# Kernel tuning notes

Measured on AMD Instinct MI355X. Metric: run time of the kernel, lower is better.

The kernel has to match this reference:

```python
import jax, jax.numpy as jnp
import numpy as np

B, L, D, H = 4, 2048, 1024, 16
HD = D // H

def setup_inputs() -> dict:
    key = jax.random.key(0)
    ks = jax.random.split(key, 11)
    s = 1.0 / np.sqrt(D)
    return {
        "query": jax.random.normal(ks[0], (B, L, D), jnp.float32),
        "key": jax.random.normal(ks[1], (B, L, D), jnp.float32),
        "value": jax.random.normal(ks[2], (B, L, D), jnp.float32),
        "Wq": jax.random.normal(ks[3], (D, D), jnp.float32) * s,
        "bq": jnp.zeros((D,), jnp.float32),
        "Wk": jax.random.normal(ks[4], (D, D), jnp.float32) * s,
        "bk": jnp.zeros((D,), jnp.float32),
        "Wv": jax.random.normal(ks[5], (D, D), jnp.float32) * s,
        "bv": jnp.zeros((D,), jnp.float32),
        "Wo": jax.random.normal(ks[6], (D, D), jnp.float32) * s,
        "bo": jnp.zeros((D,), jnp.float32),
    }

def reference(query, key, value, Wq, bq, Wk, bk, Wv, bv, Wo, bo):
    b = query.shape[0]
    # linear projections (torch Linear: x @ W.T + b)
    Q = query @ Wq.T + bq
    K = key @ Wk.T + bk
    V = value @ Wv.T + bv
    # split heads -> [b, h, l, hd]
    Q = Q.reshape(b, -1, H, HD).transpose(0, 2, 1, 3)
    K = K.reshape(b, -1, H, HD).transpose(0, 2, 1, 3)
    V = V.reshape(b, -1, H, HD).transpose(0, 2, 1, 3)
    energy = jnp.einsum('bhqd,bhkd->bhqk', Q, K) / jnp.sqrt(jnp.float32(HD))
    attn = jax.nn.softmax(energy, axis=-1)
    x = jnp.einsum('bhqk,bhkd->bhqd', attn, V)
    x = x.transpose(0, 2, 1, 3).reshape(b, -1, D)
    return x @ Wo.T + bo
```

## Files before the change

### kernel.cpp

```cpp
#include <hip/hip_runtime.h>

typedef float floatx4 __attribute__((ext_vector_type(4)));
typedef short bf16x8 __attribute__((ext_vector_type(8)));
typedef const unsigned int __attribute__((address_space(1))) gas_u32;
typedef unsigned int __attribute__((address_space(3))) las_u32;

#if __has_builtin(__builtin_amdgcn_exp2f)
#define EXP2F(x) __builtin_amdgcn_exp2f(x)
#else
#define EXP2F(x) exp2f(x)
#endif

__device__ __forceinline__ unsigned short f2bf(float x) {
    unsigned int u = __float_as_uint(x);
    unsigned int r = u + 0x7fffu + ((u >> 16) & 1u);
    return (unsigned short)(r >> 16);
}

__device__ __forceinline__ unsigned int pack2bf_t(float lo, float hi) {
    return (__float_as_uint(lo) >> 16) | (__float_as_uint(hi) & 0xffff0000u);
}

__device__ __forceinline__ void g2l16(const void* g, void* l) {
    __builtin_amdgcn_global_load_lds((gas_u32*)(unsigned long long)g,
                                     (las_u32*)(unsigned int)(unsigned long long)l,
                                     16, 0, 0);
}

__global__ __launch_bounds__(256) void cvt5_kernel(
    const float* __restrict__ k, const float* __restrict__ v,
    const float* __restrict__ wq, const float* __restrict__ wk, const float* __restrict__ wv,
    unsigned short* __restrict__ kb, unsigned short* __restrict__ vb,
    unsigned short* __restrict__ wqb, unsigned short* __restrict__ wkb,
    unsigned short* __restrict__ wvb) {
    const int ty = blockIdx.y;
    const float* src; unsigned short* dst; int n4;
    switch (ty) {
        case 0: src = k;  dst = kb;  n4 = 2097152; break;
        case 1: src = v;  dst = vb;  n4 = 2097152; break;
        case 2: src = wq; dst = wqb; n4 = 262144;  break;
        case 3: src = wk; dst = wkb; n4 = 262144;  break;
        default: src = wv; dst = wvb; n4 = 262144; break;
    }
    int i = blockIdx.x * 256 + threadIdx.x;
    if (i >= n4) return;
    float4 x = ((const float4*)src)[i];
    ushort4 o;
    o.x = f2bf(x.x); o.y = f2bf(x.y); o.z = f2bf(x.z); o.w = f2bf(x.w);
    ((ushort4*)dst)[i] = o;
}

__global__ __launch_bounds__(256) void cvt1_kernel(const float* __restrict__ wo,
                                                   unsigned short* __restrict__ wob) {
    int i = blockIdx.x * 256 + threadIdx.x;
    float4 x = ((const float4*)wo)[i];
    ushort4 o;
    o.x = f2bf(x.x); o.y = f2bf(x.y); o.z = f2bf(x.z); o.w = f2bf(x.w);
    ((ushort4*)wob)[i] = o;
}

template <int OUT_MODE, bool A_FP32>
__device__ __forceinline__ void gemm_body(const void* __restrict__ Aptr,
                                          const unsigned short* __restrict__ W,
                                          const float* __restrict__ bias,
                                          void* __restrict__ Cout,
                                          unsigned short* As, unsigned short* Bs,
                                          int m0, int n0, int N, int K, float scale) {
    const int t = threadIdx.x;
    const int lane = t & 63, w = t >> 6;
    const int lr = lane & 15, quad = lane >> 4;
    const int wm = (w & 1) * 64, wn = (w >> 1) * 64;

    const int s0 = w * 128 + lane, s1 = s0 + 64;
    const int r0 = s0 >> 2, c0 = ((s0 & 3) ^ (r0 & 3)) * 8;
    const int r1 = s1 >> 2, c1 = ((s1 & 3) ^ (r1 & 3)) * 8;
    const unsigned short* gw0 = W + (size_t)(n0 + r0) * K + c0;
    const unsigned short* gw1 = W + (size_t)(n0 + r1) * K + c1;

    const unsigned short* ga0 = nullptr;
    const unsigned short* ga1 = nullptr;
    if constexpr (!A_FP32) {
        const unsigned short* A = (const unsigned short*)Aptr;
        ga0 = A + (size_t)(m0 + r0) * K + c0;
        ga1 = A + (size_t)(m0 + r1) * K + c1;
    }

    floatx4 acc[4][4];
#pragma unroll
    for (int i = 0; i < 4; ++i)
#pragma unroll
        for (int j = 0; j < 4; ++j) acc[i][j] = (floatx4){0.f, 0.f, 0.f, 0.f};

    const int xs = (lr & 3);

    auto stageB = [&](int buf, int k0) {
        unsigned short* Bb = Bs + buf * 4096;
        g2l16(gw0 + k0, &Bb[(size_t)(w * 128) * 8]);
        g2l16(gw1 + k0, &Bb[(size_t)(w * 128 + 64) * 8]);
    };

    auto readB = [&](int buf, bf16x8* bfr, int ch) {
        const unsigned short* Bb = Bs + buf * 4096;
#pragma unroll
        for (int j = 0; j < 4; ++j)
            bfr[j] = *(const bf16x8*)&Bb[(wn + j * 16 + lr) * 32 + ch * 8];
    };

    auto mfma16 = [&](const bf16x8* af, const bf16x8* bfr) {
#pragma unroll
        for (int i = 0; i < 4; ++i)
#pragma unroll
            for (int j = 0; j < 4; ++j) {
                if constexpr (OUT_MODE == 2)
                    acc[i][j] = __builtin_amdgcn_mfma_f32_16x16x32_bf16(bfr[j], af[i], acc[i][j], 0, 0, 0);
                else
                    acc[i][j] = __builtin_amdgcn_mfma_f32_16x16x32_bf16(af[i], bfr[j], acc[i][j], 0, 0, 0);
            }
    };

    if constexpr (!A_FP32) {
        auto stageA = [&](int buf, int k0) {
            unsigned short* Ab = As + buf * 4096;
            g2l16(ga0 + k0, &Ab[(size_t)(w * 128) * 8]);
            g2l16(ga1 + k0, &Ab[(size_t)(w * 128 + 64) * 8]);
        };
        auto step = [&](int buf) {
            const unsigned short* Ab = As + buf * 4096;
            bf16x8 af[4], bfr[4];
#pragma unroll
            for (int i = 0; i < 4; ++i)
                af[i] = *(const bf16x8*)&Ab[(wm + i * 16 + lr) * 32 + ((quad ^ xs) * 8)];
            readB(buf, bfr, quad ^ xs);
            mfma16(af, bfr);
        };
        stageB(0, 0);
        stageA(0, 0);
        __syncthreads();
        for (int k0 = 0; k0 < K - 64; k0 += 64) {
            stageB(1, k0 + 32);
            stageA(1, k0 + 32);
            step(0);
            __syncthreads();
            stageB(0, k0 + 64);
            stageA(0, k0 + 64);
            step(1);
            __syncthreads();
        }
        stageB(1, K - 32);
        stageA(1, K - 32);
        step(0);
        __syncthreads();
        step(1);
    } else {
        const float* A = (const float*)Aptr;
        float4 va[4];
        auto loadA32 = [&](int k0) {
#pragma unroll
            for (int i = 0; i < 4; ++i) {
                int idx = t + 256 * i;
                int row = idx >> 3;
                int c4 = (idx & 7) * 4;
                va[i] = *(const float4*)(A + (size_t)(m0 + row) * K + k0 + c4);
            }
        };
        auto writeA32 = [&](int buf) {
            unsigned short* Ab = As + buf * 4096;
#pragma unroll
            for (int i = 0; i < 4; ++i) {
                int idx = t + 256 * i;
                int row = idx >> 3;
                int c4 = (idx & 7) * 4;
                ushort4 bv;
                bv.x = f2bf(va[i].x); bv.y = f2bf(va[i].y);
                bv.z = f2bf(va[i].z); bv.w = f2bf(va[i].w);
                *(ushort4*)&Ab[row * 32 + c4] = bv;
            }
        };
        auto stepA = [&](int buf) {
            const unsigned short* Ab = As + buf * 4096;
            bf16x8 af[4], bfr[4];
#pragma unroll
            for (int i = 0; i < 4; ++i)
                af[i] = *(const bf16x8*)&Ab[(wm + i * 16 + lr) * 32 + quad * 8];
            readB(buf, bfr, quad ^ xs);
            mfma16(af, bfr);
        };
        stageB(0, 0);
        loadA32(0);
        writeA32(0);
        __syncthreads();
        for (int k0 = 0; k0 < K - 64; k0 += 64) {
            stageB(1, k0 + 32);
            loadA32(k0 + 32);
            stepA(0);
            writeA32(1);
            __syncthreads();
            stageB(0, k0 + 64);
            loadA32(k0 + 64);
            stepA(1);
            writeA32(0);
            __syncthreads();
        }
        stageB(1, K - 32);
        loadA32(K - 32);
        stepA(0);
        writeA32(1);
        __syncthreads();
        stepA(1);
    }

    if constexpr (OUT_MODE == 2) {
        const int b = m0 >> 11;
        unsigned short* VT = (unsigned short*)Cout;
#pragma unroll
        for (int i = 0; i < 4; ++i) {
#pragma unroll
            for (int j = 0; j < 4; ++j) {
#pragma unroll
                for (int r = 0; r < 4; ++r) {
                    int d = n0 + wn + j * 16 + quad * 4 + r;
                    int tok = (m0 & 2047) + wm + i * 16 + lr;
                    float val = acc[i][j][r] + bias[d];
                    int t6 = tok & 63;
                    int ntok = (tok & ~63) | ((((t6 >> 3) ^ (d & 7)) << 3)) | (t6 & 7);
                    VT[(((size_t)b * 16 + (d >> 6)) * 64 + (d & 63)) * 2048 + ntok] = f2bf(val);
                }
            }
        }
    } else if constexpr (OUT_MODE == 3) {
        unsigned short* C = (unsigned short*)Cout;
#pragma unroll
        for (int i = 0; i < 4; ++i) {
#pragma unroll
            for (int j = 0; j < 4; ++j) {
#pragma unroll
                for (int r = 0; r < 4; ++r) {
                    int row = m0 + wm + i * 16 + quad * 4 + r;
                    int col = n0 + wn + j * 16 + lr;
                    float val = acc[i][j][r] + bias[col];
                    int r6 = row & 63;
                    int srow = (r6 & 32) | (((r6 >> 2) & 1) << 4) |
                               (((r6 >> 3) & 3) << 2) | (r6 & 3);
                    int nrow = (row & ~63) | srow;
                    int c6 = col & 63;
                    int ncol = (col & ~63) | ((((c6 >> 3) ^ (srow & 7)) << 3)) | (c6 & 7);
                    C[(size_t)nrow * N + ncol] = f2bf(val);
                }
            }
        }
    } else {
#pragma unroll
        for (int i = 0; i < 4; ++i) {
#pragma unroll
            for (int j = 0; j < 4; ++j) {
#pragma unroll
                for (int r = 0; r < 4; ++r) {
                    int row = m0 + wm + i * 16 + quad * 4 + r;
                    int col = n0 + wn + j * 16 + lr;
                    float val = (acc[i][j][r] + bias[col]) * scale;
                    if constexpr (OUT_MODE == 1)
                        ((unsigned short*)Cout)[(size_t)row * N + col] = f2bf(val);
                    else
                        ((float*)Cout)[(size_t)row * N + col] = val;
                }
            }
        }
    }
}

__device__ __forceinline__ void gemm_swz(int bx, int by, int& m0, int& n0) {
    const int hw = bx + 8 * by;
    const int wid = (hw & 7) * 64 + (hw >> 3);
    m0 = (wid >> 3) * 128;
    n0 = (wid & 7) * 128;
}

__global__ __launch_bounds__(256) void gemm_qkv(
    const float* __restrict__ query, const unsigned short* __restrict__ wqb,
    const float* __restrict__ bq, unsigned short* __restrict__ Qp,
    const unsigned short* __restrict__ kb, const unsigned short* __restrict__ wkb,
    const float* __restrict__ bk, unsigned short* __restrict__ Kp,
    const unsigned short* __restrict__ vb, const unsigned short* __restrict__ wvb,
    const float* __restrict__ bv, unsigned short* __restrict__ VTp, float qscale) {
    __shared__ unsigned short As[2 * 128 * 32];
    __shared__ unsigned short Bs[2 * 128 * 32];
    int m0, n0;
    gemm_swz(blockIdx.x, blockIdx.y, m0, n0);
    if (blockIdx.z == 0)
        gemm_body<1, true>(query, wqb, bq, Qp, As, Bs, m0, n0, 1024, 1024, qscale);
    else if (blockIdx.z == 1)
        gemm_body<3, false>(kb, wkb, bk, Kp, As, Bs, m0, n0, 1024, 1024, 1.0f);
    else
        gemm_body<2, false>(vb, wvb, bv, VTp, As, Bs, m0, n0, 1024, 1024, 1.0f);
}

__global__ __launch_bounds__(256) void gemm_o(const unsigned short* __restrict__ A,
                                              const unsigned short* __restrict__ W,
                                              const float* __restrict__ bias,
                                              void* __restrict__ C) {
    __shared__ unsigned short As[2 * 128 * 32];
    __shared__ unsigned short Bs[2 * 128 * 32];
    int m0, n0;
    gemm_swz(blockIdx.x, blockIdx.y, m0, n0);
    gemm_body<0, false>(A, W, bias, C, As, Bs, m0, n0, 1024, 1024, 1.0f);
}

__global__ __launch_bounds__(256) void attn_kernel(const unsigned short* __restrict__ Qp,
                                                   const unsigned short* __restrict__ Kp,
                                                   const unsigned short* __restrict__ VTp,
                                                   unsigned short* __restrict__ Xp) {
    constexpr int L = 2048, D = 1024;
    __shared__ unsigned short Ks[2][64 * 64];
    __shared__ unsigned short Vt[2][64 * 64];

    const int t = threadIdx.x;
    const int hw = blockIdx.x + 16 * blockIdx.y + 256 * blockIdx.z;
    const int wid = (hw & 7) * 128 + (hw >> 3);
    const int q0 = (wid & 15) * 128;
    const int h = (wid >> 4) & 15;
    const int b = wid >> 8;
    const int lane = t & 63;
    const int w = t >> 6;
    const int lr = lane & 15;
    const int quad = lane >> 4;
    const int x7 = lr & 7;

    const size_t kbase = ((size_t)(b * L)) * D + (size_t)h * 64;
    const size_t vtbase = ((size_t)(b * 16 + h)) * 64 * 2048;

    auto stage_async = [&](int buf, int kb2) {
        int k0 = kb2 * 64;
#pragma unroll
        for (int i = 0; i < 2; ++i) {
            int idx = t + 256 * i;
            int row = idx >> 3, c16 = idx & 7;
            g2l16(Kp + kbase + (size_t)(k0 + row) * D + c16 * 8,
                  &Ks[buf][(w * 64 + i * 256) * 8]);
            g2l16(VTp + vtbase + (size_t)row * 2048 + k0 + c16 * 8,
                  &Vt[buf][(w * 64 + i * 256) * 8]);
        }
    };

    stage_async(0, 0);

    const size_t qbase = ((size_t)(b * L + q0)) * D + (size_t)h * 64;
    bf16x8 bq[2][2];
#pragma unroll
    for (int qs = 0; qs < 2; ++qs)
#pragma unroll
        for (int s2 = 0; s2 < 2; ++s2)
            bq[qs][s2] = *(const bf16x8*)(Qp + qbase + (size_t)(w * 32 + qs * 16 + lr) * D +
                                          s2 * 32 + quad * 8);

    floatx4 o[2][4], ol[2];
#pragma unroll
    for (int qs = 0; qs < 2; ++qs) {
        ol[qs] = (floatx4){0.f, 0.f, 0.f, 0.f};
#pragma unroll
        for (int dt = 0; dt < 4; ++dt) o[qs][dt] = (floatx4){0.f, 0.f, 0.f, 0.f};
    }
    bf16x8 ones;
#pragma unroll
    for (int e = 0; e < 8; ++e) ones[e] = (short)0x3F80;

    __syncthreads();
    int cur = 0;

    const int kc0 = (quad ^ x7) * 8;
    const int kc1 = ((quad + 4) ^ x7) * 8;

    for (int kb = 0; kb < L / 64; ++kb) {
        if (kb < L / 64 - 1) stage_async(cur ^ 1, kb + 1);

        __builtin_amdgcn_s_setprio(1);
#pragma unroll
        for (int g = 0; g < 2; ++g) {
            bf16x8 akA0 = *(const bf16x8*)&Ks[cur][(g * 32 + lr) * 64 + kc0];
            bf16x8 akA1 = *(const bf16x8*)&Ks[cur][(g * 32 + lr) * 64 + kc1];
            bf16x8 akB0 = *(const bf16x8*)&Ks[cur][(g * 32 + 16 + lr) * 64 + kc0];
            bf16x8 akB1 = *(const bf16x8*)&Ks[cur][(g * 32 + 16 + lr) * 64 + kc1];
            bf16x8 vf[4];
#pragma unroll
            for (int dt = 0; dt < 4; ++dt)
                vf[dt] = *(const bf16x8*)&Vt[cur][(dt * 16 + lr) * 64 +
                                                  (((g * 4 + quad) ^ x7) * 8)];

            const floatx4 z4 = (floatx4){0.f, 0.f, 0.f, 0.f};
#pragma unroll
            for (int qs = 0; qs < 2; ++qs) {
                floatx4 stA = __builtin_amdgcn_mfma_f32_16x16x32_bf16(akA0, bq[qs][0], z4, 0, 0, 0);
                stA = __builtin_amdgcn_mfma_f32_16x16x32_bf16(akA1, bq[qs][1], stA, 0, 0, 0);
                floatx4 stB = __builtin_amdgcn_mfma_f32_16x16x32_bf16(akB0, bq[qs][0], z4, 0, 0, 0);
                stB = __builtin_amdgcn_mfma_f32_16x16x32_bf16(akB1, bq[qs][1], stB, 0, 0, 0);

                union { unsigned int u[4]; bf16x8 v; } pf;
                pf.u[0] = pack2bf_t(EXP2F(stA[0]), EXP2F(stA[1]));
                pf.u[1] = pack2bf_t(EXP2F(stA[2]), EXP2F(stA[3]));
                pf.u[2] = pack2bf_t(EXP2F(stB[0]), EXP2F(stB[1]));
                pf.u[3] = pack2bf_t(EXP2F(stB[2]), EXP2F(stB[3]));

                ol[qs] = __builtin_amdgcn_mfma_f32_16x16x32_bf16(pf.v, ones, ol[qs], 0, 0, 0);
#pragma unroll
                for (int dt = 0; dt < 4; ++dt)
                    o[qs][dt] = __builtin_amdgcn_mfma_f32_16x16x32_bf16(pf.v, vf[dt],
                                                                        o[qs][dt], 0, 0, 0);
            }
        }
        __builtin_amdgcn_s_setprio(0);

        if (kb < L / 64 - 1) {
            __syncthreads();
            cur ^= 1;
        }
    }

#pragma unroll
    for (int qs = 0; qs < 2; ++qs) {
#pragma unroll
        for (int r = 0; r < 4; ++r) {
            float inv = 1.0f / ol[qs][r];
            int q = q0 + w * 32 + qs * 16 + quad * 4 + r;
            size_t base = ((size_t)(b * L + q)) * D + (size_t)h * 64;
#pragma unroll
            for (int dt = 0; dt < 4; ++dt)
                Xp[base + dt * 16 + lr] = f2bf(o[qs][dt][r] * inv);
        }
    }
}

extern "C" void kernel_launch(void* const* d_in, const int* in_sizes, int n_in,
                              void* d_out, int out_size, void* d_ws, size_t ws_size,
                              hipStream_t stream) {
    const float* query = (const float*)d_in[0];
    const float* key_  = (const float*)d_in[1];
    const float* value = (const float*)d_in[2];
    const float* Wq = (const float*)d_in[3];
    const float* bq = (const float*)d_in[4];
    const float* Wk = (const float*)d_in[5];
    const float* bk = (const float*)d_in[6];
    const float* Wv = (const float*)d_in[7];
    const float* bv = (const float*)d_in[8];
    const float* Wo = (const float*)d_in[9];
    const float* bo = (const float*)d_in[10];
    float* out = (float*)d_out;

    const size_t MB16 = (size_t)8 * 1024 * 1024;

    unsigned short* Qp  = (unsigned short*)d_ws;
    unsigned short* kb  = Qp + MB16;
    unsigned short* vb  = kb + MB16;
    unsigned short* VTp = vb + MB16;
    unsigned short* Xp  = kb;
    unsigned short* wob = vb;
    unsigned short* Kp  = (unsigned short*)d_out;
    unsigned short* wqb = Kp + MB16;
    unsigned short* wkb = wqb + 1024 * 1024;
    unsigned short* wvb = wkb + 1024 * 1024;

    const float qscale = 0.125f * 1.44269504f;

    dim3 bb(256);
    cvt5_kernel<<<dim3(8192, 5), bb, 0, stream>>>(key_, value, Wq, Wk, Wv,
                                                  kb, vb, wqb, wkb, wvb);
    gemm_qkv<<<dim3(8, 64, 3), bb, 0, stream>>>(query, wqb, bq, Qp,
                                                kb, wkb, bk, Kp,
                                                vb, wvb, bv, VTp, qscale);
    attn_kernel<<<dim3(16, 16, 4), bb, 0, stream>>>(Qp, Kp, VTp, Xp);
    cvt1_kernel<<<dim3(1024), bb, 0, stream>>>(Wo, wob);
    gemm_o<<<dim3(8, 64), bb, 0, stream>>>(Xp, wob, bo, out);
}
```

Measured before the change: 338.9 us.

## Add 256x128 triple-buffered 512-thread GEMM for K/V and output projections

Adds a new bf16 GEMM body with 256x128 tiles, 512 threads, a three-stage LDS ring filled by global_load_lds, explicit vmcnt waits and raw barriers, and s_setprio around the MFMA compute. The K/V projections and the output projection now use it. The fp32-A Q projection is split into its own kernel on the old 128x128 path. The goal is to cut per-block overhead and hide global-load latency with deeper prefetch, at the cost of more LDS per block, fewer resident blocks, and an extra kernel launch.

Result: no change. 344.8 us (+1.7%).

```diff
diff --git a/kernel.cpp b/kernel.cpp
--- a/kernel.cpp
+++ b/kernel.cpp
@@ -77,14 +77,6 @@
     const unsigned short* gw0 = W + (size_t)(n0 + r0) * K + c0;
     const unsigned short* gw1 = W + (size_t)(n0 + r1) * K + c1;
 
-    const unsigned short* ga0 = nullptr;
-    const unsigned short* ga1 = nullptr;
-    if constexpr (!A_FP32) {
-        const unsigned short* A = (const unsigned short*)Aptr;
-        ga0 = A + (size_t)(m0 + r0) * K + c0;
-        ga1 = A + (size_t)(m0 + r1) * K + c1;
-    }
-
     floatx4 acc[4][4];
 #pragma unroll
     for (int i = 0; i < 4; ++i)
@@ -110,48 +102,11 @@
 #pragma unroll
         for (int i = 0; i < 4; ++i)
 #pragma unroll
-            for (int j = 0; j < 4; ++j) {
-                if constexpr (OUT_MODE == 2)
-                    acc[i][j] = __builtin_amdgcn_mfma_f32_16x16x32_bf16(bfr[j], af[i], acc[i][j], 0, 0, 0);
-                else
-                    acc[i][j] = __builtin_amdgcn_mfma_f32_16x16x32_bf16(af[i], bfr[j], acc[i][j], 0, 0, 0);
-            }
+            for (int j = 0; j < 4; ++j)
+                acc[i][j] = __builtin_amdgcn_mfma_f32_16x16x32_bf16(af[i], bfr[j], acc[i][j], 0, 0, 0);
     };
 
-    if constexpr (!A_FP32) {
-        auto stageA = [&](int buf, int k0) {
-            unsigned short* Ab = As + buf * 4096;
-            g2l16(ga0 + k0, &Ab[(size_t)(w * 128) * 8]);
-            g2l16(ga1 + k0, &Ab[(size_t)(w * 128 + 64) * 8]);
-        };
-        auto step = [&](int buf) {
-            const unsigned short* Ab = As + buf * 4096;
-            bf16x8 af[4], bfr[4];
-#pragma unroll
-            for (int i = 0; i < 4; ++i)
-                af[i] = *(const bf16x8*)&Ab[(wm + i * 16 + lr) * 32 + ((quad ^ xs) * 8)];
-            readB(buf, bfr, quad ^ xs);
-            mfma16(af, bfr);
-        };
-        stageB(0, 0);
-        stageA(0, 0);
-        __syncthreads();
-        for (int k0 = 0; k0 < K - 64; k0 += 64) {
-            stageB(1, k0 + 32);
-            stageA(1, k0 + 32);
-            step(0);
-            __syncthreads();
-            stageB(0, k0 + 64);
-            stageA(0, k0 + 64);
-            step(1);
-            __syncthreads();
-        }
-        stageB(1, K - 32);
-        stageA(1, K - 32);
-        step(0);
-        __syncthreads();
-        step(1);
-    } else {
+    {
         const float* A = (const float*)Aptr;
         float4 va[4];
         auto loadA32 = [&](int k0) {
@@ -209,6 +164,126 @@
         stepA(1);
     }
 
+#pragma unroll
+    for (int i = 0; i < 4; ++i) {
+#pragma unroll
+        for (int j = 0; j < 4; ++j) {
+#pragma unroll
+            for (int r = 0; r < 4; ++r) {
+                int row = m0 + wm + i * 16 + quad * 4 + r;
+                int col = n0 + wn + j * 16 + lr;
+                float val = (acc[i][j][r] + bias[col]) * scale;
+                ((unsigned short*)Cout)[(size_t)row * N + col] = f2bf(val);
+            }
+        }
+    }
+}
+
+__device__ __forceinline__ void gemm_swz(int bx, int by, int& m0, int& n0) {
+    const int hw = bx + 8 * by;
+    const int wid = (hw & 7) * 64 + (hw >> 3);
+    m0 = (wid >> 3) * 128;
+    n0 = (wid & 7) * 128;
+}
+
+__global__ __launch_bounds__(256) void gemm_q(
+    const float* __restrict__ query, const unsigned short* __restrict__ wqb,
+    const float* __restrict__ bq, unsigned short* __restrict__ Qp, float qscale) {
+    __shared__ unsigned short As[2 * 128 * 32];
+    __shared__ unsigned short Bs[2 * 128 * 32];
+    int m0, n0;
+    gemm_swz(blockIdx.x, blockIdx.y, m0, n0);
+    gemm_body<1, true>(query, wqb, bq, Qp, As, Bs, m0, n0, 1024, 1024, qscale);
+}
+
+template <int OUT_MODE>
+__device__ __forceinline__ void gemm256_body(const unsigned short* __restrict__ Asrc,
+                                             const unsigned short* __restrict__ W,
+                                             const float* __restrict__ bias,
+                                             void* __restrict__ Cout,
+                                             unsigned short* lds, int m0, int n0) {
+    constexpr int K = 1024, N = 1024;
+    const int t = threadIdx.x;
+    const int lane = t & 63, w = t >> 6;
+    const int lr = lane & 15, quad = lane >> 4;
+    const int wrow = (w & 3) * 64, wcol = (w >> 2) * 64;
+
+    const unsigned short* gA[4];
+    const unsigned short* gB[2];
+#pragma unroll
+    for (int i = 0; i < 4; ++i) {
+        int idx = t + 512 * i;
+        int row = idx >> 3, sl = idx & 7;
+        gA[i] = Asrc + (size_t)(m0 + row) * K + ((sl ^ (row & 7)) * 8);
+    }
+#pragma unroll
+    for (int i = 0; i < 2; ++i) {
+        int idx = t + 512 * i;
+        int row = idx >> 3, sl = idx & 7;
+        gB[i] = W + (size_t)(n0 + row) * K + ((sl ^ (row & 7)) * 8);
+    }
+
+    auto STAGE = [&](int buf, int kt) {
+        unsigned short* dst = lds + buf * 24576;
+#pragma unroll
+        for (int i = 0; i < 4; ++i)
+            g2l16(gA[i] + kt * 64, dst + (w * 64 + i * 512) * 8);
+#pragma unroll
+        for (int i = 0; i < 2; ++i)
+            g2l16(gB[i] + kt * 64, dst + 16384 + (w * 64 + i * 512) * 8);
+    };
+
+    floatx4 acc[4][4];
+#pragma unroll
+    for (int i = 0; i < 4; ++i)
+#pragma unroll
+        for (int j = 0; j < 4; ++j) acc[i][j] = (floatx4){0.f, 0.f, 0.f, 0.f};
+
+    const int sc0 = (quad ^ (lr & 7)) * 8;
+    const int sc1 = sc0 ^ 32;
+
+    auto COMPUTE = [&](int buf) {
+        const unsigned short* Ab = lds + buf * 24576;
+        const unsigned short* Bb = Ab + 16384;
+#pragma unroll
+        for (int kh = 0; kh < 2; ++kh) {
+            const int sc = kh ? sc1 : sc0;
+            bf16x8 af[4], bfr[4];
+#pragma unroll
+            for (int i = 0; i < 4; ++i)
+                af[i] = *(const bf16x8*)&Ab[(wrow + i * 16 + lr) * 64 + sc];
+#pragma unroll
+            for (int j = 0; j < 4; ++j)
+                bfr[j] = *(const bf16x8*)&Bb[(wcol + j * 16 + lr) * 64 + sc];
+#pragma unroll
+            for (int i = 0; i < 4; ++i)
+#pragma unroll
+                for (int j = 0; j < 4; ++j) {
+                    if constexpr (OUT_MODE == 2)
+                        acc[i][j] = __builtin_amdgcn_mfma_f32_16x16x32_bf16(bfr[j], af[i], acc[i][j], 0, 0, 0);
+                    else
+                        acc[i][j] = __builtin_amdgcn_mfma_f32_16x16x32_bf16(af[i], bfr[j], acc[i][j], 0, 0, 0);
+                }
+        }
+    };
+
+    STAGE(0, 0);
+    STAGE(1, 1);
+    for (int kt = 0; kt < 16; ++kt) {
+        if (kt < 15) {
+            asm volatile("s_waitcnt vmcnt(6)" ::: "memory");
+        } else {
+            asm volatile("s_waitcnt vmcnt(0)" ::: "memory");
+        }
+        __builtin_amdgcn_sched_barrier(0);
+        __builtin_amdgcn_s_barrier();
+        __builtin_amdgcn_sched_barrier(0);
+        if (kt + 2 < 16) STAGE((kt + 2) % 3, kt + 2);
+        __builtin_amdgcn_s_setprio(1);
+        COMPUTE(kt % 3);
+        __builtin_amdgcn_s_setprio(0);
+    }
+
     if constexpr (OUT_MODE == 2) {
         const int b = m0 >> 11;
         unsigned short* VT = (unsigned short*)Cout;
@@ -218,8 +293,8 @@
             for (int j = 0; j < 4; ++j) {
 #pragma unroll
                 for (int r = 0; r < 4; ++r) {
-                    int d = n0 + wn + j * 16 + quad * 4 + r;
-                    int tok = (m0 & 2047) + wm + i * 16 + lr;
+                    int d = n0 + wcol + j * 16 + quad * 4 + r;
+                    int tok = (m0 & 2047) + wrow + i * 16 + lr;
                     float val = acc[i][j][r] + bias[d];
                     int t6 = tok & 63;
                     int ntok = (tok & ~63) | ((((t6 >> 3) ^ (d & 7)) << 3)) | (t6 & 7);
@@ -235,8 +310,8 @@
             for (int j = 0; j < 4; ++j) {
 #pragma unroll
                 for (int r = 0; r < 4; ++r) {
-                    int row = m0 + wm + i * 16 + quad * 4 + r;
-                    int col = n0 + wn + j * 16 + lr;
+                    int row = m0 + wrow + i * 16 + quad * 4 + r;
+                    int col = n0 + wcol + j * 16 + lr;
                     float val = acc[i][j][r] + bias[col];
                     int r6 = row & 63;
                     int srow = (r6 & 32) | (((r6 >> 2) & 1) << 4) |
@@ -255,54 +330,43 @@
             for (int j = 0; j < 4; ++j) {
 #pragma unroll
                 for (int r = 0; r < 4; ++r) {
-                    int row = m0 + wm + i * 16 + quad * 4 + r;
-                    int col = n0 + wn + j * 16 + lr;
-                    float val = (acc[i][j][r] + bias[col]) * scale;
-                    if constexpr (OUT_MODE == 1)
-                        ((unsigned short*)Cout)[(size_t)row * N + col] = f2bf(val);
-                    else
-                        ((float*)Cout)[(size_t)row * N + col] = val;
+                    int row = m0 + wrow + i * 16 + quad * 4 + r;
+                    int col = n0 + wcol + j * 16 + lr;
+                    ((float*)Cout)[(size_t)row * N + col] = acc[i][j][r] + bias[col];
                 }
             }
         }
     }
 }
 
-__device__ __forceinline__ void gemm_swz(int bx, int by, int& m0, int& n0) {
-    const int hw = bx + 8 * by;
-    const int wid = (hw & 7) * 64 + (hw >> 3);
-    m0 = (wid >> 3) * 128;
+__device__ __forceinline__ void gemm_swz256(int bx, int& m0, int& n0) {
+    const int wid = (bx & 7) * 32 + (bx >> 3);
+    m0 = (wid >> 3) * 256;
     n0 = (wid & 7) * 128;
 }
 
-__global__ __launch_bounds__(256) void gemm_qkv(
-    const float* __restrict__ query, const unsigned short* __restrict__ wqb,
-    const float* __restrict__ bq, unsigned short* __restrict__ Qp,
+__global__ __launch_bounds__(512) void gemm_kv(
     const unsigned short* __restrict__ kb, const unsigned short* __restrict__ wkb,
     const float* __restrict__ bk, unsigned short* __restrict__ Kp,
     const unsigned short* __restrict__ vb, const unsigned short* __restrict__ wvb,
-    const float* __restrict__ bv, unsigned short* __restrict__ VTp, float qscale) {
-    __shared__ unsigned short As[2 * 128 * 32];
-    __shared__ unsigned short Bs[2 * 128 * 32];
+    const float* __restrict__ bv, unsigned short* __restrict__ VTp) {
+    __shared__ unsigned short lds[3 * 24576];
     int m0, n0;
-    gemm_swz(blockIdx.x, blockIdx.y, m0, n0);
+    gemm_swz256(blockIdx.x, m0, n0);
     if (blockIdx.z == 0)
-        gemm_body<1, true>(query, wqb, bq, Qp, As, Bs, m0, n0, 1024, 1024, qscale);
-    else if (blockIdx.z == 1)
-        gemm_body<3, false>(kb, wkb, bk, Kp, As, Bs, m0, n0, 1024, 1024, 1.0f);
+        gemm256_body<3>(kb, wkb, bk, Kp, lds, m0, n0);
     else
-        gemm_body<2, false>(vb, wvb, bv, VTp, As, Bs, m0, n0, 1024, 1024, 1.0f);
-}
-
-__global__ __launch_bounds__(256) void gemm_o(const unsigned short* __restrict__ A,
+        gemm256_body<2>(vb, wvb, bv, VTp, lds, m0, n0);
+}
+
+__global__ __launch_bounds__(512) void gemm_o(const unsigned short* __restrict__ A,
                                               const unsigned short* __restrict__ W,
                                               const float* __restrict__ bias,
                                               void* __restrict__ C) {
-    __shared__ unsigned short As[2 * 128 * 32];
-    __shared__ unsigned short Bs[2 * 128 * 32];
+    __shared__ unsigned short lds[3 * 24576];
     int m0, n0;
-    gemm_swz(blockIdx.x, blockIdx.y, m0, n0);
-    gemm_body<0, false>(A, W, bias, C, As, Bs, m0, n0, 1024, 1024, 1.0f);
+    gemm_swz256(blockIdx.x, m0, n0);
+    gemm256_body<0>(A, W, bias, C, lds, m0, n0);
 }
 
 __global__ __launch_bounds__(256) void attn_kernel(const unsigned short* __restrict__ Qp,
@@ -462,10 +526,10 @@
     dim3 bb(256);
     cvt5_kernel<<<dim3(8192, 5), bb, 0, stream>>>(key_, value, Wq, Wk, Wv,
                                                   kb, vb, wqb, wkb, wvb);
-    gemm_qkv<<<dim3(8, 64, 3), bb, 0, stream>>>(query, wqb, bq, Qp,
-                                                kb, wkb, bk, Kp,
-                                                vb, wvb, bv, VTp, qscale);
+    gemm_q<<<dim3(8, 64), bb, 0, stream>>>(query, wqb, bq, Qp, qscale);
+    gemm_kv<<<dim3(256, 1, 2), dim3(512), 0, stream>>>(kb, wkb, bk, Kp,
+                                                       vb, wvb, bv, VTp);
     attn_kernel<<<dim3(16, 16, 4), bb, 0, stream>>>(Qp, Kp, VTp, Xp);
     cvt1_kernel<<<dim3(1024), bb, 0, stream>>>(Wo, wob);
-    gemm_o<<<dim3(8, 64), bb, 0, stream>>>(Xp, wob, bo, out);
-}
+    gemm_o<<<dim3(256), dim3(512), 0, stream>>>(Xp, wob, bo, out);
+}
```
